# Kernel optimization log

Measured on AMD Instinct MI355X. Metric: run time of the kernel, lower is better.

## Reference

```python
import jax, jax.numpy as jnp
import numpy as np

DIM = 128
CODEBOOK_SIZE = 1024
DECAY = 0.99
EPSILON = 1e-06


def setup_inputs() -> dict:
    key = jax.random.key(0)
    k1, k2, k3, k4 = jax.random.split(key, 4)
    x = jax.random.normal(k1, (64, 1024, DIM), dtype=jnp.float32)
    embed = jax.random.normal(k2, (CODEBOOK_SIZE, DIM), dtype=jnp.float32)
    # keep all codes above the dead-code threshold (2) so expire_codes_ is a no-op
    cluster_size = jax.random.uniform(k3, (CODEBOOK_SIZE,), dtype=jnp.float32) * 10.0 + 2.0
    embed_avg = jax.random.normal(k4, (CODEBOOK_SIZE, DIM), dtype=jnp.float32)
    return {"x": x, "embed": embed, "cluster_size": cluster_size, "embed_avg": embed_avg}


def reference(x, embed, cluster_size, embed_avg):
    shape = x.shape
    xf = x.reshape(-1, shape[-1])  # [N, D]

    # quantize: squared euclidean distances [N, K] then argmin
    dist = (
        jnp.sum(xf * xf, axis=1, keepdims=True)
        - 2.0 * (xf @ embed.T)
        + jnp.sum(embed * embed, axis=1)[None, :]
    )
    embed_ind_flat = jnp.argmin(dist, axis=-1)  # [N]
    embed_ind = embed_ind_flat.reshape(shape[:-1])

    # dequantize
    quantize = embed[embed_ind]  # [..., D]

    # training EMA updates (one-hot scatter accumulation)
    one_hot_sum = jax.ops.segment_sum(
        jnp.ones_like(embed_ind_flat, dtype=x.dtype), embed_ind_flat,
        num_segments=CODEBOOK_SIZE)
    embed_sum = jax.ops.segment_sum(xf, embed_ind_flat, num_segments=CODEBOOK_SIZE)  # [K, D]

    cluster_size_new = cluster_size * DECAY + one_hot_sum * (1.0 - DECAY)
    embed_avg_new = embed_avg * DECAY + embed_sum * (1.0 - DECAY)

    total = jnp.sum(cluster_size_new)
    smoothed = (cluster_size_new + EPSILON) / (total + EPSILON * CODEBOOK_SIZE) * total
    embed_new = embed_avg_new / smoothed[:, None]

    return quantize, embed_ind, cluster_size_new, embed_avg_new, embed_new
```

## Files before the change

### kernel.cpp

```cpp
#include <hip/hip_runtime.h>
#include <float.h>

#define DIMD   128
#define KCODES 1024
#define NROWS  65536
#define TAU    0.012f
#define SEG_R  8

typedef __attribute__((ext_vector_type(8)))  short short8;
typedef __attribute__((ext_vector_type(16))) float f32x16;

union U8 { uint4 u; short8 s; };

__device__ __forceinline__ unsigned bfr(float f) {
    unsigned u = __float_as_uint(f);
    return (u + 0x7fffu + ((u >> 16) & 1u)) >> 16;
}

__global__ __launch_bounds__(256) void pre_kernel(
    const float* __restrict__ embed, uint4* __restrict__ ehg, uint4* __restrict__ elg,
    float* __restrict__ enorm, uint4* __restrict__ zero_region)
{
    if (blockIdx.x < 64) {
        int t = blockIdx.x * 256 + threadIdx.x;
        int chunk = t >> 9;
        int s = (t >> 6) & 7;
        int L = t & 63;
        const float* src = embed + ((size_t)(chunk * 32 + (L & 31)) * DIMD) + s * 16 + (L >> 5) * 8;
        float4 a = *(const float4*)src;
        float4 b = *(const float4*)(src + 4);
        float f[8] = {a.x, a.y, a.z, a.w, b.x, b.y, b.z, b.w};
        unsigned hi[8], lo[8];
#pragma unroll
        for (int j = 0; j < 8; ++j) {
            hi[j] = bfr(f[j]);
            float hf = __uint_as_float(hi[j] << 16);
            lo[j] = bfr(f[j] - hf);
        }
        uint4 H, Lw;
        H.x = hi[0] | (hi[1] << 16); H.y = hi[2] | (hi[3] << 16);
        H.z = hi[4] | (hi[5] << 16); H.w = hi[6] | (hi[7] << 16);
        Lw.x = lo[0] | (lo[1] << 16); Lw.y = lo[2] | (lo[3] << 16);
        Lw.z = lo[4] | (lo[5] << 16); Lw.w = lo[6] | (lo[7] << 16);
        ehg[t] = H;
        elg[t] = Lw;
    } else if (blockIdx.x < 68) {
        int k = (blockIdx.x - 64) * 256 + threadIdx.x;
        const float4* e = (const float4*)(embed + (size_t)k * DIMD);
        float s = 0.f;
#pragma unroll
        for (int c = 0; c < DIMD / 4; ++c) {
            float4 v = e[c];
            s += v.x * v.x + v.y * v.y + v.z * v.z + v.w * v.w;
        }
        enorm[k] = s;
    } else {
        uint4 z = {0, 0, 0, 0};
        zero_region[threadIdx.x] = z;
        zero_region[threadIdx.x + 256] = z;
    }
}

__global__ __launch_bounds__(256, 2) void argmin_mfma(
    const float* __restrict__ x, const uint4* __restrict__ ehg, const uint4* __restrict__ elg,
    const float* __restrict__ enorm,
    int* __restrict__ ind_i, float* __restrict__ ind_f,
    int* __restrict__ wl, int* __restrict__ wl_cnt, int* __restrict__ counts)
{
    __shared__ uint4 Bs[1024];

    const int tid  = threadIdx.x;
    const int wave = tid >> 6;
    const int lane = tid & 63;
    const int n    = lane & 31;
    const int h    = lane >> 5;
    const int row0 = blockIdx.x * 128;
    const int rowA = row0 + wave * 32 + n;

    uint4 xh[8], xl[8];
    const float* xrow = x + (size_t)rowA * DIMD + h * 8;
#pragma unroll
    for (int s = 0; s < 8; ++s) {
        float4 a = *(const float4*)(xrow + s * 16);
        float4 b = *(const float4*)(xrow + s * 16 + 4);
        float f[8] = {a.x, a.y, a.z, a.w, b.x, b.y, b.z, b.w};
        unsigned hi[8], lo[8];
#pragma unroll
        for (int j = 0; j < 8; ++j) {
            hi[j] = bfr(f[j]);
            float hf = __uint_as_float(hi[j] << 16);
            lo[j] = bfr(f[j] - hf);
        }
        xh[s].x = hi[0] | (hi[1] << 16); xh[s].y = hi[2] | (hi[3] << 16);
        xh[s].z = hi[4] | (hi[5] << 16); xh[s].w = hi[6] | (hi[7] << 16);
        xl[s].x = lo[0] | (lo[1] << 16); xl[s].y = lo[2] | (lo[3] << 16);
        xl[s].z = lo[4] | (lo[5] << 16); xl[s].w = lo[6] | (lo[7] << 16);
    }

    float bestv[16], best2[16];
    int   besti[16];
#pragma unroll
    for (int r = 0; r < 16; ++r) { bestv[r] = FLT_MAX; best2[r] = FLT_MAX; besti[r] = 0; }

    for (int chunk = 0; chunk < KCODES / 32; ++chunk) {
        __syncthreads();
        {
            const uint4* sh = ehg + chunk * 512;
            const uint4* sl = elg + chunk * 512;
#pragma unroll
            for (int i = 0; i < 2; ++i) {
                int idx = tid + i * 256;
                Bs[idx]       = sh[idx];
                Bs[512 + idx] = sl[idx];
            }
        }
        float ee_val = enorm[chunk * 32 + n];
        __syncthreads();

        f32x16 acc;
#pragma unroll
        for (int r = 0; r < 16; ++r) acc[r] = 0.f;

#pragma unroll
        for (int s = 0; s < 8; ++s) {
            U8 ah, al, bh, bl;
            ah.u = xh[s]; al.u = xl[s];
            bh.u = Bs[s * 64 + lane];
            bl.u = Bs[512 + s * 64 + lane];
            acc = __builtin_amdgcn_mfma_f32_32x32x16_bf16(ah.s, bh.s, acc, 0, 0, 0);
            acc = __builtin_amdgcn_mfma_f32_32x32x16_bf16(ah.s, bl.s, acc, 0, 0, 0);
            acc = __builtin_amdgcn_mfma_f32_32x32x16_bf16(al.s, bh.s, acc, 0, 0, 0);
        }

        const int nglob = chunk * 32 + n;
#pragma unroll
        for (int r = 0; r < 16; ++r) {
            float d = fmaf(-2.f, acc[r], ee_val);
            bool c1 = d < bestv[r];
            float t = c1 ? bestv[r] : d;
            best2[r] = fminf(best2[r], t);
            besti[r] = c1 ? nglob : besti[r];
            bestv[r] = fminf(bestv[r], d);
        }
    }

#pragma unroll
    for (int m = 1; m <= 16; m <<= 1) {
#pragma unroll
        for (int r = 0; r < 16; ++r) {
            float ov = __shfl_xor(bestv[r], m, 64);
            float o2 = __shfl_xor(best2[r], m, 64);
            int   oi = __shfl_xor(besti[r], m, 64);
            float hi = fmaxf(bestv[r], ov);
            best2[r] = fminf(fminf(best2[r], o2), hi);
            bool take = (ov < bestv[r]) || (ov == bestv[r] && oi < besti[r]);
            bestv[r] = take ? ov : bestv[r];
            besti[r] = take ? oi : besti[r];
        }
    }

    if (n == 0) {
#pragma unroll
        for (int r = 0; r < 16; ++r) {
            int row = row0 + wave * 32 + (r & 3) + 8 * (r >> 2) + 4 * h;
            ind_i[row] = besti[r];
            ind_f[row] = (float)besti[r];
            atomicAdd(&counts[besti[r]], 1);
            if (best2[r] - bestv[r] < TAU) {
                int p = atomicAdd(wl_cnt, 1);
                wl[p] = row;
            }
        }
    }
}

__global__ __launch_bounds__(256) void recheck_kernel(
    const float* __restrict__ x, const float* __restrict__ embed,
    const float* __restrict__ enorm, const int* __restrict__ wl,
    const int* __restrict__ wl_cnt, int* __restrict__ ind_i, float* __restrict__ ind_f,
    int* __restrict__ counts)
{
    __shared__ float xs[DIMD];
    __shared__ float rv[256];
    __shared__ int   ri[256];
    const int tid = threadIdx.x;
    const int count = *wl_cnt;

    for (int i = blockIdx.x; i < count; i += gridDim.x) {
        const int row = wl[i];
        __syncthreads();
        if (tid < DIMD) xs[tid] = x[(size_t)row * DIMD + tid];
        __syncthreads();

        const float4* xs4 = (const float4*)xs;
        float xn = 0.f;
#pragma unroll 8
        for (int c = 0; c < 32; ++c) {
            float4 v = xs4[c];
            xn += v.x * v.x + v.y * v.y + v.z * v.z + v.w * v.w;
        }

        float bv = FLT_MAX; int bi = 0;
#pragma unroll
        for (int c = 0; c < 4; ++c) {
            int code = tid * 4 + c;
            const float4* er = (const float4*)(embed + (size_t)code * DIMD);
            float acc = 0.f;
#pragma unroll 8
            for (int kk = 0; kk < 32; ++kk) {
                float4 a = xs4[kk];
                float4 b = er[kk];
                acc += a.x * b.x + a.y * b.y + a.z * b.z + a.w * b.w;
            }
            float d = (xn - 2.0f * acc) + enorm[code];
            if (d < bv) { bv = d; bi = code; }
        }
        rv[tid] = bv; ri[tid] = bi;
        __syncthreads();
        for (int s = 128; s > 0; s >>= 1) {
            if (tid < s) {
                if (rv[tid + s] < rv[tid] || (rv[tid + s] == rv[tid] && ri[tid + s] < ri[tid])) {
                    rv[tid] = rv[tid + s]; ri[tid] = ri[tid + s];
                }
            }
            __syncthreads();
        }
        if (tid == 0) {
            int s_new = ri[0];
            int s_old = ind_i[row];
            if (s_new != s_old) {
                ind_i[row] = s_new;
                ind_f[row] = (float)s_new;
                atomicAdd(&counts[s_old], -1);
                atomicAdd(&counts[s_new], 1);
            }
        }
        __syncthreads();
    }
}

__global__ __launch_bounds__(1024) void scan_cluster_kernel(
    const int* __restrict__ counts, const float* __restrict__ cluster_size,
    int* __restrict__ cursor, float* __restrict__ out_cs, float* __restrict__ smoothed)
{
    __shared__ int   s[KCODES];
    __shared__ float rf[KCODES];
    const int t = threadIdx.x;
    int my = counts[t];
    s[t] = my;
    float cs = cluster_size[t] * 0.99f + (float)my * 0.01f;
    out_cs[t] = cs;
    rf[t] = cs;
    __syncthreads();
    for (int d = 1; d < KCODES; d <<= 1) {
        int v = (t >= d) ? s[t - d] : 0;
        __syncthreads();
        s[t] += v;
        __syncthreads();
    }
    cursor[t] = s[t] - my;
    for (int st = 512; st > 0; st >>= 1) {
        if (t < st) rf[t] += rf[t + st];
        __syncthreads();
    }
    float total = rf[0];
    smoothed[t] = (cs + 1e-6f) / (total + 1e-6f * (float)KCODES) * total;
}

__global__ __launch_bounds__(256) void permbuild_kernel(
    const int* __restrict__ ind, int* __restrict__ cursor,
    int* __restrict__ perm, int* __restrict__ codes, uint4* __restrict__ embed_sum4)
{
    const int tid = threadIdx.x;
    if (tid < 128) {
        uint4 z = {0, 0, 0, 0};
        embed_sum4[blockIdx.x * 128 + tid] = z;
    }
    const int row = blockIdx.x * 256 + tid;
    const int k = ind[row];
    int pos = atomicAdd(&cursor[k], 1);
    perm[pos] = row;
    codes[pos] = k;
}

__global__ __launch_bounds__(256) void segsum_kernel(
    const float* __restrict__ x, const float* __restrict__ embed,
    const int* __restrict__ perm, const int* __restrict__ codes,
    float* __restrict__ embed_sum, float* __restrict__ out_q)
{
    const int g = (blockIdx.x * 256 + threadIdx.x) >> 5;
    const int c = threadIdx.x & 31;
    const int base = g * SEG_R;

    float4 acc = {0.f, 0.f, 0.f, 0.f};
    int curk = codes[base];
#pragma unroll
    for (int j = 0; j < SEG_R; ++j) {
        int r = perm[base + j];
        int k = codes[base + j];
        float4 v = *(const float4*)(x + (size_t)r * DIMD + c * 4);
        float4 e = *(const float4*)(embed + (size_t)k * DIMD + c * 4);
        *(float4*)(out_q + (size_t)r * DIMD + c * 4) = e;
        if (k != curk) {
            float* dst = embed_sum + (size_t)curk * DIMD + c * 4;
            atomicAdd(dst + 0, acc.x);
            atomicAdd(dst + 1, acc.y);
            atomicAdd(dst + 2, acc.z);
            atomicAdd(dst + 3, acc.w);
            acc = v;
            curk = k;
        } else {
            acc.x += v.x; acc.y += v.y; acc.z += v.z; acc.w += v.w;
        }
    }
    float* dst = embed_sum + (size_t)curk * DIMD + c * 4;
    atomicAdd(dst + 0, acc.x);
    atomicAdd(dst + 1, acc.y);
    atomicAdd(dst + 2, acc.z);
    atomicAdd(dst + 3, acc.w);
}

__global__ void embed_kernel(
    const float* __restrict__ embed_avg, const float* __restrict__ embed_sum,
    const float* __restrict__ smoothed, float* __restrict__ out_ea,
    float* __restrict__ out_en)
{
    int i = blockIdx.x * blockDim.x + threadIdx.x;
    if (i < KCODES * DIMD) {
        float ea = embed_avg[i] * 0.99f + embed_sum[i] * 0.01f;
        out_ea[i] = ea;
        out_en[i] = ea / smoothed[i >> 7];
    }
}

extern "C" void kernel_launch(void* const* d_in, const int* in_sizes, int n_in,
                              void* d_out, int out_size, void* d_ws, size_t ws_size,
                              hipStream_t stream) {
    const float* x            = (const float*)d_in[0];
    const float* embed        = (const float*)d_in[1];
    const float* cluster_size = (const float*)d_in[2];
    const float* embed_avg    = (const float*)d_in[3];

    float* out     = (float*)d_out;
    float* out_q   = out;
    float* out_ind = out + 8388608;
    float* out_cs  = out + 8454144;
    float* out_ea  = out + 8455168;
    float* out_en  = out + 8586240;

    char* ws = (char*)d_ws;
    int*   ind_i     = (int*)(ws + 0);
    float* enorm     = (float*)(ws + 262144);
    int*   countsI   = (int*)(ws + 266240);
    int*   wl_cnt    = (int*)(ws + 270336);
    int*   cursor    = (int*)(ws + 274432);
    float* smoothed  = (float*)(ws + 278528);
    int*   perm      = (int*)(ws + 286720);
    int*   wl        = (int*)(ws + 548864);
    int*   codes     = (int*)(ws + 548864);
    uint4* ehg       = (uint4*)(ws + 811008);
    uint4* elg       = (uint4*)(ws + 1073152);
    float* embed_sum = (float*)(ws + 811008);

    pre_kernel<<<69, 256, 0, stream>>>(embed, ehg, elg, enorm, (uint4*)countsI);
    argmin_mfma<<<NROWS / 128, 256, 0, stream>>>(
        x, ehg, elg, enorm, ind_i, out_ind, wl, wl_cnt, countsI);
    recheck_kernel<<<256, 256, 0, stream>>>(
        x, embed, enorm, wl, wl_cnt, ind_i, out_ind, countsI);
    scan_cluster_kernel<<<1, 1024, 0, stream>>>(countsI, cluster_size, cursor, out_cs, smoothed);
    permbuild_kernel<<<NROWS / 256, 256, 0, stream>>>(
        ind_i, cursor, perm, codes, (uint4*)embed_sum);
    segsum_kernel<<<(NROWS / SEG_R) * 32 / 256, 256, 0, stream>>>(
        x, embed, perm, codes, embed_sum, out_q);
    embed_kernel<<<(KCODES * DIMD + 255) / 256, 256, 0, stream>>>(
        embed_avg, embed_sum, smoothed, out_ea, out_en);
}
```

Measured before the change: 290.0 us.

## Switch argmin MFMA to fp16 split with two products and separate histogram

Replaces the three-product bf16 hi/lo split of x and the codebook with fp16, using an fp16 codebook and an fp16 hi/lo split of x only, which cuts MFMA work and codebook shared-memory traffic by about a third. The near-tie threshold for exact fp32 rechecking is widened to make up for the lower precision of the embedding. Per-row global atomic count updates are removed from argmin and recheck and replaced by a separate shared-memory histogram kernel. Occupancy hint is raised to 3 blocks and recheck grid doubled; SEG_R is increased. The tradeoffs are more rows on the recheck worklist and a risk of fp16 range issues.

```diff
diff --git a/kernel.cpp b/kernel.cpp
--- a/kernel.cpp
+++ b/kernel.cpp
@@ -1,24 +1,25 @@
 #include <hip/hip_runtime.h>
+#include <hip/hip_fp16.h>
 #include <float.h>
 
 #define DIMD   128
 #define KCODES 1024
 #define NROWS  65536
-#define TAU    0.012f
-#define SEG_R  8
-
-typedef __attribute__((ext_vector_type(8)))  short short8;
+#define TAU    0.03f
+#define SEG_R  16
+
+typedef __attribute__((ext_vector_type(8)))  _Float16 half8;
 typedef __attribute__((ext_vector_type(16))) float f32x16;
 
-union U8 { uint4 u; short8 s; };
-
-__device__ __forceinline__ unsigned bfr(float f) {
-    unsigned u = __float_as_uint(f);
-    return (u + 0x7fffu + ((u >> 16) & 1u)) >> 16;
+union U8 { uint4 u; half8 h; };
+
+__device__ __forceinline__ unsigned packh2(float a, float b) {
+    __half2 t = __floats2half2_rn(a, b);
+    return *(unsigned*)&t;
 }
 
 __global__ __launch_bounds__(256) void pre_kernel(
-    const float* __restrict__ embed, uint4* __restrict__ ehg, uint4* __restrict__ elg,
+    const float* __restrict__ embed, uint4* __restrict__ ehg,
     float* __restrict__ enorm, uint4* __restrict__ zero_region)
 {
     if (blockIdx.x < 64) {
@@ -30,20 +31,11 @@
         float4 a = *(const float4*)src;
         float4 b = *(const float4*)(src + 4);
         float f[8] = {a.x, a.y, a.z, a.w, b.x, b.y, b.z, b.w};
-        unsigned hi[8], lo[8];
-#pragma unroll
-        for (int j = 0; j < 8; ++j) {
-            hi[j] = bfr(f[j]);
-            float hf = __uint_as_float(hi[j] << 16);
-            lo[j] = bfr(f[j] - hf);
-        }
-        uint4 H, Lw;
-        H.x = hi[0] | (hi[1] << 16); H.y = hi[2] | (hi[3] << 16);
-        H.z = hi[4] | (hi[5] << 16); H.w = hi[6] | (hi[7] << 16);
-        Lw.x = lo[0] | (lo[1] << 16); Lw.y = lo[2] | (lo[3] << 16);
-        Lw.z = lo[4] | (lo[5] << 16); Lw.w = lo[6] | (lo[7] << 16);
+        uint4 H;
+        unsigned* hw = (unsigned*)&H;
+#pragma unroll
+        for (int j = 0; j < 4; ++j) hw[j] = packh2(f[2 * j], f[2 * j + 1]);
         ehg[t] = H;
-        elg[t] = Lw;
     } else if (blockIdx.x < 68) {
         int k = (blockIdx.x - 64) * 256 + threadIdx.x;
         const float4* e = (const float4*)(embed + (size_t)k * DIMD);
@@ -61,13 +53,13 @@
     }
 }
 
-__global__ __launch_bounds__(256, 2) void argmin_mfma(
-    const float* __restrict__ x, const uint4* __restrict__ ehg, const uint4* __restrict__ elg,
+__global__ __launch_bounds__(256, 3) void argmin_mfma(
+    const float* __restrict__ x, const uint4* __restrict__ ehg,
     const float* __restrict__ enorm,
     int* __restrict__ ind_i, float* __restrict__ ind_f,
-    int* __restrict__ wl, int* __restrict__ wl_cnt, int* __restrict__ counts)
-{
-    __shared__ uint4 Bs[1024];
+    int* __restrict__ wl, int* __restrict__ wl_cnt)
+{
+    __shared__ uint4 Bs[512];
 
     const int tid  = threadIdx.x;
     const int wave = tid >> 6;
@@ -84,17 +76,17 @@
         float4 a = *(const float4*)(xrow + s * 16);
         float4 b = *(const float4*)(xrow + s * 16 + 4);
         float f[8] = {a.x, a.y, a.z, a.w, b.x, b.y, b.z, b.w};
-        unsigned hi[8], lo[8];
-#pragma unroll
-        for (int j = 0; j < 8; ++j) {
-            hi[j] = bfr(f[j]);
-            float hf = __uint_as_float(hi[j] << 16);
-            lo[j] = bfr(f[j] - hf);
-        }
-        xh[s].x = hi[0] | (hi[1] << 16); xh[s].y = hi[2] | (hi[3] << 16);
-        xh[s].z = hi[4] | (hi[5] << 16); xh[s].w = hi[6] | (hi[7] << 16);
-        xl[s].x = lo[0] | (lo[1] << 16); xl[s].y = lo[2] | (lo[3] << 16);
-        xl[s].z = lo[4] | (lo[5] << 16); xl[s].w = lo[6] | (lo[7] << 16);
+        unsigned* ph = (unsigned*)&xh[s];
+        unsigned* pl = (unsigned*)&xl[s];
+#pragma unroll
+        for (int j = 0; j < 4; ++j) {
+            float u0 = f[2 * j], u1 = f[2 * j + 1];
+            __half2 hh = __floats2half2_rn(u0, u1);
+            ph[j] = *(unsigned*)&hh;
+            float2 back = __half22float2(hh);
+            __half2 ll = __floats2half2_rn(u0 - back.x, u1 - back.y);
+            pl[j] = *(unsigned*)&ll;
+        }
     }
 
     float bestv[16], best2[16];
@@ -106,13 +98,8 @@
         __syncthreads();
         {
             const uint4* sh = ehg + chunk * 512;
-            const uint4* sl = elg + chunk * 512;
-#pragma unroll
-            for (int i = 0; i < 2; ++i) {
-                int idx = tid + i * 256;
-                Bs[idx]       = sh[idx];
-                Bs[512 + idx] = sl[idx];
-            }
+            Bs[tid]       = sh[tid];
+            Bs[tid + 256] = sh[tid + 256];
         }
         float ee_val = enorm[chunk * 32 + n];
         __syncthreads();
@@ -123,13 +110,11 @@
 
 #pragma unroll
         for (int s = 0; s < 8; ++s) {
-            U8 ah, al, bh, bl;
+            U8 ah, al, bh;
             ah.u = xh[s]; al.u = xl[s];
             bh.u = Bs[s * 64 + lane];
-            bl.u = Bs[512 + s * 64 + lane];
-            acc = __builtin_amdgcn_mfma_f32_32x32x16_bf16(ah.s, bh.s, acc, 0, 0, 0);
-            acc = __builtin_amdgcn_mfma_f32_32x32x16_bf16(ah.s, bl.s, acc, 0, 0, 0);
-            acc = __builtin_amdgcn_mfma_f32_32x32x16_bf16(al.s, bh.s, acc, 0, 0, 0);
+            acc = __builtin_amdgcn_mfma_f32_32x32x16_f16(ah.h, bh.h, acc, 0, 0, 0);
+            acc = __builtin_amdgcn_mfma_f32_32x32x16_f16(al.h, bh.h, acc, 0, 0, 0);
         }
 
         const int nglob = chunk * 32 + n;
@@ -165,10 +150,9 @@
             int row = row0 + wave * 32 + (r & 3) + 8 * (r >> 2) + 4 * h;
             ind_i[row] = besti[r];
             ind_f[row] = (float)besti[r];
-            atomicAdd(&counts[besti[r]], 1);
             if (best2[r] - bestv[r] < TAU) {
                 int p = atomicAdd(wl_cnt, 1);
-                wl[p] = row;
+                if (p < NROWS) wl[p] = row;
             }
         }
     }
@@ -177,14 +161,14 @@
 __global__ __launch_bounds__(256) void recheck_kernel(
     const float* __restrict__ x, const float* __restrict__ embed,
     const float* __restrict__ enorm, const int* __restrict__ wl,
-    const int* __restrict__ wl_cnt, int* __restrict__ ind_i, float* __restrict__ ind_f,
-    int* __restrict__ counts)
+    const int* __restrict__ wl_cnt, int* __restrict__ ind_i, float* __restrict__ ind_f)
 {
     __shared__ float xs[DIMD];
     __shared__ float rv[256];
     __shared__ int   ri[256];
     const int tid = threadIdx.x;
-    const int count = *wl_cnt;
+    int count = *wl_cnt;
+    if (count > NROWS) count = NROWS;
 
     for (int i = blockIdx.x; i < count; i += gridDim.x) {
         const int row = wl[i];
@@ -227,15 +211,27 @@
         }
         if (tid == 0) {
             int s_new = ri[0];
-            int s_old = ind_i[row];
-            if (s_new != s_old) {
+            if (s_new != ind_i[row]) {
                 ind_i[row] = s_new;
                 ind_f[row] = (float)s_new;
-                atomicAdd(&counts[s_old], -1);
-                atomicAdd(&counts[s_new], 1);
             }
         }
         __syncthreads();
+    }
+}
+
+__global__ __launch_bounds__(256) void hist_kernel(
+    const int* __restrict__ ind, int* __restrict__ counts)
+{
+    __shared__ int hcnt[KCODES];
+    for (int i = threadIdx.x; i < KCODES; i += 256) hcnt[i] = 0;
+    __syncthreads();
+    const int base = blockIdx.x * 2048;
+    for (int i = threadIdx.x; i < 2048; i += 256) atomicAdd(&hcnt[ind[base + i]], 1);
+    __syncthreads();
+    for (int i = threadIdx.x; i < KCODES; i += 256) {
+        int v = hcnt[i];
+        if (v) atomicAdd(&counts[i], v);
     }
 }
 
@@ -359,14 +355,14 @@
     int*   wl        = (int*)(ws + 548864);
     int*   codes     = (int*)(ws + 548864);
     uint4* ehg       = (uint4*)(ws + 811008);
-    uint4* elg       = (uint4*)(ws + 1073152);
     float* embed_sum = (float*)(ws + 811008);
 
-    pre_kernel<<<69, 256, 0, stream>>>(embed, ehg, elg, enorm, (uint4*)countsI);
+    pre_kernel<<<69, 256, 0, stream>>>(embed, ehg, enorm, (uint4*)countsI);
     argmin_mfma<<<NROWS / 128, 256, 0, stream>>>(
-        x, ehg, elg, enorm, ind_i, out_ind, wl, wl_cnt, countsI);
-    recheck_kernel<<<256, 256, 0, stream>>>(
-        x, embed, enorm, wl, wl_cnt, ind_i, out_ind, countsI);
+        x, ehg, enorm, ind_i, out_ind, wl, wl_cnt);
+    recheck_kernel<<<512, 256, 0, stream>>>(
+        x, embed, enorm, wl, wl_cnt, ind_i, out_ind);
+    hist_kernel<<<32, 256, 0, stream>>>(ind_i, countsI);
     scan_cluster_kernel<<<1, 1024, 0, stream>>>(countsI, cluster_size, cursor, out_cs, smoothed);
     permbuild_kernel<<<NROWS / 256, 256, 0, stream>>>(
         ind_i, cursor, perm, codes, (uint4*)embed_sum);
```

Result: slower. 394.6 us (+36.1%).
